# Performance work log

Measured on AMD Instinct MI355X. Metric: run time of the kernel, lower is better.

## Reference

```python
import jax, jax.numpy as jnp
import numpy as np

N = 8192
IN_F = 512
OUT_F = 512
ALPHA = 0.2  # leaky relu slope


def setup_inputs() -> dict:
    key = jax.random.key(0)
    k1, k2, k3, k4, k5 = jax.random.split(key, 5)
    inp = jax.random.normal(k1, (N, IN_F), dtype=jnp.float32)
    adj = jax.random.randint(k2, (N, N), 0, 2, dtype=jnp.int32)
    # linear1: [in, out] + bias
    W1 = jax.random.normal(k3, (IN_F, OUT_F), dtype=jnp.float32) * (1.0 / np.sqrt(IN_F))
    b1 = jnp.zeros((OUT_F,), dtype=jnp.float32)
    # linear2: maps 2*out -> 1; split into the two halves acting on h_i and h_j
    a = jax.random.normal(k4, (2 * OUT_F,), dtype=jnp.float32) * (1.0 / np.sqrt(2 * OUT_F))
    a1 = a[:OUT_F]
    a2 = a[OUT_F:]
    b2 = jnp.zeros((), dtype=jnp.float32)
    return {"inp": inp, "adj": adj, "W1": W1, "b1": b1, "a1": a1, "a2": a2, "b2": b2}


def reference(inp, adj, W1, b1, a1, a2, b2):
    h = inp @ W1 + b1  # [N, out]
    # linear2(cat(h_i, h_j)) == h_i@a1 + h_j@a2 + b2 -> avoids the N*N*2F tensor
    e = jax.nn.leaky_relu((h @ a1)[:, None] + (h @ a2)[None, :] + b2, ALPHA)  # [N, N]
    attention = jnp.where(adj > 0, e, jnp.float32(-1e12))
    attention = jax.nn.softmax(attention, axis=1)
    h_prime = attention @ h  # [N, out]
    return jax.nn.elu(h_prime)  # concat=True
```

## Files before the change

kernel.cpp:

```cpp
#include <hip/hip_runtime.h>
#include <hip/hip_bf16.h>
#include <stdint.h>

#define NR 8192
#define FD 512
#define BM 64

typedef __attribute__((ext_vector_type(8))) short s8v;
typedef __attribute__((ext_vector_type(4))) float f32x4;

static __device__ __forceinline__ short bf16_rtne(float x) {
    union { float f; uint32_t u; } v; v.f = x;
    uint32_t r = (v.u + 0x7FFFu + ((v.u >> 16) & 1u)) >> 16;
    return (short)r;
}
static __device__ __forceinline__ float bf16_to_f32(short s) {
    union { uint32_t u; float f; } v; v.u = ((uint32_t)(uint16_t)s) << 16;
    return v.f;
}

__global__ void k_prep(const float* __restrict__ in, short* __restrict__ out,
                       const float* __restrict__ W1, short* __restrict__ W1T) {
    int b = blockIdx.x;
    if (b < 4096) {
        int i = b * 256 + threadIdx.x;
        float4 v = ((const float4*)in)[i];
        short4 s;
        s.x = bf16_rtne(v.x); s.y = bf16_rtne(v.y);
        s.z = bf16_rtne(v.z); s.w = bf16_rtne(v.w);
        ((short4*)out)[i] = s;
    } else {
        int i = (b - 4096) * 256 + threadIdx.x;
        int k = i & 511, n = i >> 9;
        W1T[(size_t)n * 512 + k] = bf16_rtne(W1[(size_t)k * 512 + n]);
    }
}

__launch_bounds__(256)
__global__ void k_gemm_h(const short* __restrict__ A,
                         const short* __restrict__ BT,
                         const float* __restrict__ b1,
                         short* __restrict__ H,
                         short* __restrict__ HT3)
{
    const int lane = threadIdx.x & 63;
    const int wn   = threadIdx.x >> 6;
    const int m    = lane & 15;
    const int q    = lane >> 4;
    const int r0   = blockIdx.x * 32;
    const int c0   = blockIdx.y * 128 + wn * 32;

    f32x4 acc[2][2] = {};
#pragma unroll 1
    for (int k0 = 0; k0 < 512; k0 += 32) {
        s8v a[2], b[2];
#pragma unroll
        for (int rt = 0; rt < 2; ++rt)
            a[rt] = *(const s8v*)(A + (size_t)(r0 + rt * 16 + m) * 512 + k0 + q * 8);
#pragma unroll
        for (int nt = 0; nt < 2; ++nt)
            b[nt] = *(const s8v*)(BT + (size_t)(c0 + nt * 16 + m) * 512 + k0 + q * 8);
#pragma unroll
        for (int rt = 0; rt < 2; ++rt)
#pragma unroll
            for (int nt = 0; nt < 2; ++nt)
                acc[rt][nt] = __builtin_amdgcn_mfma_f32_16x16x32_bf16(a[rt], b[nt], acc[rt][nt], 0, 0, 0);
    }
    float b1v[2];
#pragma unroll
    for (int nt = 0; nt < 2; ++nt) b1v[nt] = b1[c0 + nt * 16 + m];

#pragma unroll
    for (int rt = 0; rt < 2; ++rt)
#pragma unroll
        for (int nt = 0; nt < 2; ++nt) {
            int col = c0 + nt * 16 + m;
            short4 hp;
#pragma unroll
            for (int r = 0; r < 4; ++r) {
                int row = r0 + rt * 16 + q * 4 + r;
                short hv = bf16_rtne(acc[rt][nt][r] + b1v[nt]);
                H[(size_t)row * 512 + col] = hv;
                ((short*)&hp)[r] = hv;
            }
            size_t off = (size_t)blockIdx.x * 16384
                       + (size_t)(blockIdx.y * 2 + (wn >> 1)) * 2048
                       + (size_t)((wn * 2 + nt) & 3) * 512
                       + (rt * 2 + (q >> 1)) * 128
                       + m * 8 + (q & 1) * 4;
            *(short4*)(HT3 + off) = hp;
        }
}

__global__ void k_f1f2(const short* __restrict__ H, const float* __restrict__ a1,
                       const float* __restrict__ a2, const float* __restrict__ b2,
                       float* __restrict__ f1, float* __restrict__ f2s)
{
    const int lane = threadIdx.x & 63;
    const int row  = blockIdx.x * 4 + (threadIdx.x >> 6);
    s8v hv = *(const s8v*)(H + (size_t)row * 512 + lane * 8);
    float4 a1l = ((const float4*)(a1 + lane * 8))[0];
    float4 a1h = ((const float4*)(a1 + lane * 8))[1];
    float4 a2l = ((const float4*)(a2 + lane * 8))[0];
    float4 a2h = ((const float4*)(a2 + lane * 8))[1];
    float hf[8];
#pragma unroll
    for (int i = 0; i < 8; ++i) hf[i] = bf16_to_f32(hv[i]);
    float s1 = hf[0] * a1l.x + hf[1] * a1l.y + hf[2] * a1l.z + hf[3] * a1l.w
             + hf[4] * a1h.x + hf[5] * a1h.y + hf[6] * a1h.z + hf[7] * a1h.w;
    float s2 = hf[0] * a2l.x + hf[1] * a2l.y + hf[2] * a2l.z + hf[3] * a2l.w
             + hf[4] * a2h.x + hf[5] * a2h.y + hf[6] * a2h.z + hf[7] * a2h.w;
#pragma unroll
    for (int o = 32; o > 0; o >>= 1) {
        s1 += __shfl_xor(s1, o);
        s2 += __shfl_xor(s2, o);
    }
    if (lane == 0) {
        f1[row]  = s1;
        f2s[row] = s2 + b2[0];
    }
}

__launch_bounds__(1024, 4)
__global__ void k_attn(const int* __restrict__ adj,
                       const short* __restrict__ HT3,
                       const float* __restrict__ f1,
                       const float* __restrict__ f2s,
                       float* __restrict__ nump,
                       float* __restrict__ denomp)
{
    __shared__ __align__(16) short wt[2][BM * 256];

    const int t    = threadIdx.x;
    const int lane = t & 63;
    const int w    = t >> 6;
    const int m    = lane & 15;
    const int q    = lane >> 4;

    const int js   = blockIdx.x & 1;
    const int band = blockIdx.x >> 1;
    const int r0   = band * BM;
    const int jb0  = js * 4096;
    const int jt0  = js * 128;

    const int prow = t >> 4;
    const int jg   = t & 15;

    const float f1v = f1[r0 + prow];
    const int* adjrow = adj + (size_t)(r0 + prow) * NR + jb0;
    const float* f2base = f2s + jb0;

    f32x4 acc[4][2] = {};
    float dsum = 0.f;

#define GAT_BLOAD(DST, KT)                                                     \
    {                                                                          \
        const short* s_ = HT3 + (size_t)(jt0 + (KT)) * 16384 + (w >> 1) * 2048 \
                        + (w & 1) * 1024 + q * 128 + m * 8;                    \
        DST[0] = *(const s8v*)(s_);                                            \
        DST[1] = *(const s8v*)(s_ + 512);                                      \
    }

#define GAT_MLOAD(DST, AP, U)                                                  \
    {                                                                          \
        uint4 ma_ = *(const uint4*)((AP) + (U) * 8);                           \
        uint4 mb_ = *(const uint4*)((AP) + (U) * 8 + 4);                       \
        DST = ((int)ma_.x > 0 ? 1u : 0u)  | ((int)ma_.y > 0 ? 2u : 0u)         \
            | ((int)ma_.z > 0 ? 4u : 0u)  | ((int)ma_.w > 0 ? 8u : 0u)         \
            | ((int)mb_.x > 0 ? 16u : 0u) | ((int)mb_.y > 0 ? 32u : 0u)        \
            | ((int)mb_.z > 0 ? 64u : 0u) | ((int)mb_.w > 0 ? 128u : 0u);      \
    }

#define GAT_WUNIT(U, BYTE, FA, FB, P)                                          \
    {                                                                          \
        s8v wv_;                                                               \
        const float* ff_ = (const float*)&(FA);                                \
        _Pragma("unroll")                                                      \
        for (int jj = 0; jj < 4; ++jj) {                                       \
            float s_ = f1v + ff_[jj];                                          \
            float e_ = __expf(fmaxf(s_, 0.2f * s_));                           \
            float x_ = (((BYTE) >> jj) & 1u) ? e_ : 0.f;                       \
            dsum += x_; wv_[jj] = bf16_rtne(x_);                               \
        }                                                                      \
        const float* fg_ = (const float*)&(FB);                               \
        _Pragma("unroll")                                                      \
        for (int jj = 0; jj < 4; ++jj) {                                       \
            float s_ = f1v + fg_[jj];                                          \
            float e_ = __expf(fmaxf(s_, 0.2f * s_));                           \
            float x_ = (((BYTE) >> (4 + jj)) & 1u) ? e_ : 0.f;                 \
            dsum += x_; wv_[4 + jj] = bf16_rtne(x_);                           \
        }                                                                      \
        *(s8v*)&wt[P][prow * 256 + (((U) ^ (prow & 7)) << 3)] = wv_;           \
    }

    {
#pragma unroll
        for (int k_ = 0; k_ < 2; ++k_) {
            const int u_ = jg + 16 * k_;
            uint32_t mk_;
            GAT_MLOAD(mk_, adjrow, u_)
            float4 fa_ = *(const float4*)(f2base + u_ * 8);
            float4 fb_ = *(const float4*)(f2base + u_ * 8 + 4);
            GAT_WUNIT(u_, mk_, fa_, fb_, 0)
        }
    }
    s8v breg[2][2];
    GAT_BLOAD(breg[0], 0)
    GAT_BLOAD(breg[1], 1)
    __syncthreads();

    int kt = 0;
#pragma unroll 1
    for (int ch = 0; ch < 16; ++ch) {
        const int p = ch & 1;
        const int chn = (ch + 1) & 15;
        const int* adjn = adjrow + chn * 256;
        const float* f2n = f2base + chn * 256;
        uint32_t mkn_[2];
        float4 fan_[2], fbn_[2];

#pragma unroll
        for (int kk = 0; kk < 8; ++kk, ++kt) {
            const int e = kk & 1;
            s8v bn[2];
            GAT_BLOAD(bn, (kt + 2) & 127)
            if (kk < 2 && ch < 15) {
                const int u_ = jg + 16 * kk;
                GAT_MLOAD(mkn_[kk], adjn, u_)
                fan_[kk] = *(const float4*)(f2n + u_ * 8);
                fbn_[kk] = *(const float4*)(f2n + u_ * 8 + 4);
            }
            s8v af[4];
#pragma unroll
            for (int i = 0; i < 4; ++i)
                af[i] = *(const s8v*)&wt[p][(i * 16 + m) * 256
                                            + (((kk * 4 + q) ^ (m & 7)) << 3)];
#pragma unroll
            for (int nt = 0; nt < 2; ++nt)
#pragma unroll
                for (int i = 0; i < 4; ++i)
                    acc[i][nt] = __builtin_amdgcn_mfma_f32_16x16x32_bf16(af[i], breg[e][nt], acc[i][nt], 0, 0, 0);
            if (kk >= 4 && kk <= 5 && ch < 15) {
                const int k_ = kk - 4;
                const int u_ = jg + 16 * k_;
                GAT_WUNIT(u_, mkn_[k_], fan_[k_], fbn_[k_], p ^ 1)
            }
#pragma unroll
            for (int nt = 0; nt < 2; ++nt) breg[e][nt] = bn[nt];
        }
        __syncthreads();
    }
#undef GAT_BLOAD
#undef GAT_MLOAD
#undef GAT_WUNIT

    dsum += __shfl_xor(dsum, 1);
    dsum += __shfl_xor(dsum, 2);
    dsum += __shfl_xor(dsum, 4);
    dsum += __shfl_xor(dsum, 8);
    if (jg == 0) denomp[(size_t)js * NR + r0 + prow] = dsum;

    float* np = nump + (size_t)js * NR * FD;
#pragma unroll
    for (int i = 0; i < 4; ++i)
#pragma unroll
        for (int nt = 0; nt < 2; ++nt)
#pragma unroll
            for (int r = 0; r < 4; ++r) {
                int row = r0 + i * 16 + q * 4 + r;
                int col = w * 32 + nt * 16 + m;
                np[(size_t)row * FD + col] = acc[i][nt][r];
            }
}

__global__ void k_combine(const float* __restrict__ nump,
                          const float* __restrict__ denomp,
                          float* __restrict__ out)
{
    size_t e = ((size_t)blockIdx.x * 256 + threadIdx.x) * 4;
    int row = (int)(e >> 9);
    float4 n0 = *(const float4*)(nump + e);
    float4 n1 = *(const float4*)(nump + (size_t)NR * FD + e);
    float d = denomp[row] + denomp[NR + row];
    float inv = 1.0f / d;
    float4 o;
    o.x = (n0.x + n1.x) * inv;
    o.y = (n0.y + n1.y) * inv;
    o.z = (n0.z + n1.z) * inv;
    o.w = (n0.w + n1.w) * inv;
    o.x = (o.x > 0.f) ? o.x : (__expf(o.x) - 1.f);
    o.y = (o.y > 0.f) ? o.y : (__expf(o.y) - 1.f);
    o.z = (o.z > 0.f) ? o.z : (__expf(o.z) - 1.f);
    o.w = (o.w > 0.f) ? o.w : (__expf(o.w) - 1.f);
    *(float4*)(out + e) = o;
}

extern "C" void kernel_launch(void* const* d_in, const int* in_sizes, int n_in,
                              void* d_out, int out_size, void* d_ws, size_t ws_size,
                              hipStream_t stream) {
    const float* inp = (const float*)d_in[0];
    const int*   adj = (const int*)d_in[1];
    const float* W1  = (const float*)d_in[2];
    const float* b1  = (const float*)d_in[3];
    const float* a1  = (const float*)d_in[4];
    const float* a2  = (const float*)d_in[5];
    const float* b2  = (const float*)d_in[6];
    float* out = (float*)d_out;

    short*    inp_bf = (short*)d_ws;
    short*    w1t    = inp_bf + (size_t)NR * FD;
    short*    h      = w1t + (size_t)FD * FD;
    short*    ht3    = h + (size_t)NR * FD;
    float*    f1     = (float*)(ht3 + (size_t)FD * NR);
    float*    f2s    = f1 + NR;
    float*    nump   = f2s + NR;
    float*    denomp = nump + (size_t)2 * NR * FD;

    k_prep<<<4096 + 1024, 256, 0, stream>>>(inp, inp_bf, W1, w1t);
    dim3 g1(NR / 32, FD / 128);
    k_gemm_h<<<g1, 256, 0, stream>>>(inp_bf, w1t, b1, h, ht3);
    k_f1f2<<<NR / 4, 256, 0, stream>>>(h, a1, a2, b2, f1, f2s);
    k_attn<<<128 * 2, 1024, 0, stream>>>(adj, ht3, f1, f2s, nump, denomp);
    k_combine<<<(NR * FD / 4) / 256, 256, 0, stream>>>(nump, denomp, out);
}
```

Baseline: 459.7 us.

## Split attention into separate weight-generation and GEMM kernels via global bf16 buffer

The fused attention kernel is split in two. A new k_wgen kernel reads the adjacency matrix, computes the masked exp weights in bf16 in a pre-swizzled layout, and writes them to a global N×N workspace along with the full per-row denominator. k_agemm then streams those weights into shared memory and runs only the MFMA GEMM. This takes the exp and mask work off the GEMM's critical path and spreads it across many small blocks. In exchange it adds a 128 MB bf16 write plus a read-back through HBM and one extra kernel launch.

```diff
diff --git a/kernel.cpp b/kernel.cpp
--- a/kernel.cpp
+++ b/kernel.cpp
@@ -4,7 +4,6 @@
 
 #define NR 8192
 #define FD 512
-#define BM 64
 
 typedef __attribute__((ext_vector_type(8))) short s8v;
 typedef __attribute__((ext_vector_type(4))) float f32x4;
@@ -121,15 +120,92 @@
     }
 }
 
-__launch_bounds__(1024, 4)
-__global__ void k_attn(const int* __restrict__ adj,
-                       const short* __restrict__ HT3,
+__launch_bounds__(256)
+__global__ void k_wgen(const int* __restrict__ adj,
                        const float* __restrict__ f1,
                        const float* __restrict__ f2s,
-                       float* __restrict__ nump,
+                       short* __restrict__ wsw,
                        float* __restrict__ denomp)
 {
-    __shared__ __align__(16) short wt[2][BM * 256];
+    const int t    = threadIdx.x;
+    const int prow = t >> 5;
+    const int jg   = t & 31;
+    const int row  = blockIdx.x * 8 + prow;
+    const int band = row >> 6;
+    const int prow64 = row & 63;
+
+    const float f1v = f1[row];
+    const int* adjrow = adj + (size_t)row * NR;
+    short* wbase = wsw + ((size_t)(band * 32) * 64 + prow64) * 256
+                 + ((jg ^ (prow64 & 7)) << 3);
+
+    float dsum = 0.f;
+
+#define WG_COMPUTE(CH, MA, MB, FA, FB)                                         \
+    {                                                                          \
+        uint32_t bm_ =                                                         \
+              ((int)(MA).x > 0 ? 1u : 0u)   | ((int)(MA).y > 0 ? 2u : 0u)      \
+            | ((int)(MA).z > 0 ? 4u : 0u)   | ((int)(MA).w > 0 ? 8u : 0u)      \
+            | ((int)(MB).x > 0 ? 16u : 0u)  | ((int)(MB).y > 0 ? 32u : 0u)     \
+            | ((int)(MB).z > 0 ? 64u : 0u)  | ((int)(MB).w > 0 ? 128u : 0u);   \
+        s8v wv_;                                                               \
+        const float* ff_ = (const float*)&(FA);                                \
+        _Pragma("unroll")                                                      \
+        for (int jj = 0; jj < 4; ++jj) {                                       \
+            float s_ = f1v + ff_[jj];                                          \
+            float e_ = __expf(fmaxf(s_, 0.2f * s_));                           \
+            float x_ = ((bm_ >> jj) & 1u) ? e_ : 0.f;                          \
+            dsum += x_; wv_[jj] = bf16_rtne(x_);                               \
+        }                                                                      \
+        const float* fg_ = (const float*)&(FB);                                \
+        _Pragma("unroll")                                                      \
+        for (int jj = 0; jj < 4; ++jj) {                                       \
+            float s_ = f1v + fg_[jj];                                          \
+            float e_ = __expf(fmaxf(s_, 0.2f * s_));                           \
+            float x_ = ((bm_ >> (4 + jj)) & 1u) ? e_ : 0.f;                    \
+            dsum += x_; wv_[4 + jj] = bf16_rtne(x_);                           \
+        }                                                                      \
+        *(s8v*)(wbase + (size_t)(CH) * 16384) = wv_;                           \
+    }
+
+    uint4 ca, cb; float4 cf0, cf1;
+    ca  = *(const uint4*)(adjrow + jg * 8);
+    cb  = *(const uint4*)(adjrow + jg * 8 + 4);
+    cf0 = *(const float4*)(f2s + jg * 8);
+    cf1 = *(const float4*)(f2s + jg * 8 + 4);
+#pragma unroll 1
+    for (int c2 = 0; c2 < 16; ++c2) {
+        const int ch = c2 * 2;
+        uint4 na, nb; float4 nf0, nf1;
+        na  = *(const uint4*)(adjrow + (ch + 1) * 256 + jg * 8);
+        nb  = *(const uint4*)(adjrow + (ch + 1) * 256 + jg * 8 + 4);
+        nf0 = *(const float4*)(f2s + (ch + 1) * 256 + jg * 8);
+        nf1 = *(const float4*)(f2s + (ch + 1) * 256 + jg * 8 + 4);
+        WG_COMPUTE(ch, ca, cb, cf0, cf1)
+        if (c2 < 15) {
+            ca  = *(const uint4*)(adjrow + (ch + 2) * 256 + jg * 8);
+            cb  = *(const uint4*)(adjrow + (ch + 2) * 256 + jg * 8 + 4);
+            cf0 = *(const float4*)(f2s + (ch + 2) * 256 + jg * 8);
+            cf1 = *(const float4*)(f2s + (ch + 2) * 256 + jg * 8 + 4);
+        }
+        WG_COMPUTE(ch + 1, na, nb, nf0, nf1)
+    }
+#undef WG_COMPUTE
+
+    dsum += __shfl_xor(dsum, 1);
+    dsum += __shfl_xor(dsum, 2);
+    dsum += __shfl_xor(dsum, 4);
+    dsum += __shfl_xor(dsum, 8);
+    dsum += __shfl_xor(dsum, 16);
+    if (jg == 0) denomp[row] = dsum;
+}
+
+__launch_bounds__(1024, 4)
+__global__ void k_agemm(const short* __restrict__ WSW,
+                        const short* __restrict__ HT3,
+                        float* __restrict__ nump)
+{
+    __shared__ __align__(16) short wt[2][16384];
 
     const int t    = threadIdx.x;
     const int lane = t & 63;
@@ -139,19 +215,10 @@
 
     const int js   = blockIdx.x & 1;
     const int band = blockIdx.x >> 1;
-    const int r0   = band * BM;
-    const int jb0  = js * 4096;
+    const int r0   = band * 64;
     const int jt0  = js * 128;
 
-    const int prow = t >> 4;
-    const int jg   = t & 15;
-
-    const float f1v = f1[r0 + prow];
-    const int* adjrow = adj + (size_t)(r0 + prow) * NR + jb0;
-    const float* f2base = f2s + jb0;
-
     f32x4 acc[4][2] = {};
-    float dsum = 0.f;
 
 #define GAT_BLOAD(DST, KT)                                                     \
     {                                                                          \
@@ -161,48 +228,13 @@
         DST[1] = *(const s8v*)(s_ + 512);                                      \
     }
 
-#define GAT_MLOAD(DST, AP, U)                                                  \
-    {                                                                          \
-        uint4 ma_ = *(const uint4*)((AP) + (U) * 8);                           \
-        uint4 mb_ = *(const uint4*)((AP) + (U) * 8 + 4);                       \
-        DST = ((int)ma_.x > 0 ? 1u : 0u)  | ((int)ma_.y > 0 ? 2u : 0u)         \
-            | ((int)ma_.z > 0 ? 4u : 0u)  | ((int)ma_.w > 0 ? 8u : 0u)         \
-            | ((int)mb_.x > 0 ? 16u : 0u) | ((int)mb_.y > 0 ? 32u : 0u)        \
-            | ((int)mb_.z > 0 ? 64u : 0u) | ((int)mb_.w > 0 ? 128u : 0u);      \
-    }
-
-#define GAT_WUNIT(U, BYTE, FA, FB, P)                                          \
-    {                                                                          \
-        s8v wv_;                                                               \
-        const float* ff_ = (const float*)&(FA);                                \
-        _Pragma("unroll")                                                      \
-        for (int jj = 0; jj < 4; ++jj) {                                       \
-            float s_ = f1v + ff_[jj];                                          \
-            float e_ = __expf(fmaxf(s_, 0.2f * s_));                           \
-            float x_ = (((BYTE) >> jj) & 1u) ? e_ : 0.f;                       \
-            dsum += x_; wv_[jj] = bf16_rtne(x_);                               \
-        }                                                                      \
-        const float* fg_ = (const float*)&(FB);                               \
-        _Pragma("unroll")                                                      \
-        for (int jj = 0; jj < 4; ++jj) {                                       \
-            float s_ = f1v + fg_[jj];                                          \
-            float e_ = __expf(fmaxf(s_, 0.2f * s_));                           \
-            float x_ = (((BYTE) >> (4 + jj)) & 1u) ? e_ : 0.f;                 \
-            dsum += x_; wv_[4 + jj] = bf16_rtne(x_);                           \
-        }                                                                      \
-        *(s8v*)&wt[P][prow * 256 + (((U) ^ (prow & 7)) << 3)] = wv_;           \
-    }
+    const short* wsrc = WSW + (size_t)(band * 32 + js * 16) * 16384;
 
     {
-#pragma unroll
-        for (int k_ = 0; k_ < 2; ++k_) {
-            const int u_ = jg + 16 * k_;
-            uint32_t mk_;
-            GAT_MLOAD(mk_, adjrow, u_)
-            float4 fa_ = *(const float4*)(f2base + u_ * 8);
-            float4 fb_ = *(const float4*)(f2base + u_ * 8 + 4);
-            GAT_WUNIT(u_, mk_, fa_, fb_, 0)
-        }
+        s8v s0 = *(const s8v*)(wsrc + t * 16);
+        s8v s1 = *(const s8v*)(wsrc + t * 16 + 8);
+        *(s8v*)&wt[0][t * 16]     = s0;
+        *(s8v*)&wt[0][t * 16 + 8] = s1;
     }
     s8v breg[2][2];
     GAT_BLOAD(breg[0], 0)
@@ -213,23 +245,18 @@
 #pragma unroll 1
     for (int ch = 0; ch < 16; ++ch) {
         const int p = ch & 1;
-        const int chn = (ch + 1) & 15;
-        const int* adjn = adjrow + chn * 256;
-        const float* f2n = f2base + chn * 256;
-        uint32_t mkn_[2];
-        float4 fan_[2], fbn_[2];
+        s8v sg0, sg1;
+        if (ch < 15) {
+            const short* ws = wsrc + (size_t)(ch + 1) * 16384;
+            sg0 = *(const s8v*)(ws + t * 16);
+            sg1 = *(const s8v*)(ws + t * 16 + 8);
+        }
 
 #pragma unroll
         for (int kk = 0; kk < 8; ++kk, ++kt) {
             const int e = kk & 1;
             s8v bn[2];
             GAT_BLOAD(bn, (kt + 2) & 127)
-            if (kk < 2 && ch < 15) {
-                const int u_ = jg + 16 * kk;
-                GAT_MLOAD(mkn_[kk], adjn, u_)
-                fan_[kk] = *(const float4*)(f2n + u_ * 8);
-                fbn_[kk] = *(const float4*)(f2n + u_ * 8 + 4);
-            }
             s8v af[4];
 #pragma unroll
             for (int i = 0; i < 4; ++i)
@@ -240,25 +267,16 @@
 #pragma unroll
                 for (int i = 0; i < 4; ++i)
                     acc[i][nt] = __builtin_amdgcn_mfma_f32_16x16x32_bf16(af[i], breg[e][nt], acc[i][nt], 0, 0, 0);
-            if (kk >= 4 && kk <= 5 && ch < 15) {
-                const int k_ = kk - 4;
-                const int u_ = jg + 16 * k_;
-                GAT_WUNIT(u_, mkn_[k_], fan_[k_], fbn_[k_], p ^ 1)
-            }
 #pragma unroll
             for (int nt = 0; nt < 2; ++nt) breg[e][nt] = bn[nt];
         }
+        if (ch < 15) {
+            *(s8v*)&wt[p ^ 1][t * 16]     = sg0;
+            *(s8v*)&wt[p ^ 1][t * 16 + 8] = sg1;
+        }
         __syncthreads();
     }
 #undef GAT_BLOAD
-#undef GAT_MLOAD
-#undef GAT_WUNIT
-
-    dsum += __shfl_xor(dsum, 1);
-    dsum += __shfl_xor(dsum, 2);
-    dsum += __shfl_xor(dsum, 4);
-    dsum += __shfl_xor(dsum, 8);
-    if (jg == 0) denomp[(size_t)js * NR + r0 + prow] = dsum;
 
     float* np = nump + (size_t)js * NR * FD;
 #pragma unroll
@@ -281,7 +299,7 @@
     int row = (int)(e >> 9);
     float4 n0 = *(const float4*)(nump + e);
     float4 n1 = *(const float4*)(nump + (size_t)NR * FD + e);
-    float d = denomp[row] + denomp[NR + row];
+    float d = denomp[row];
     float inv = 1.0f / d;
     float4 o;
     o.x = (n0.x + n1.x) * inv;
@@ -313,13 +331,15 @@
     short*    ht3    = h + (size_t)NR * FD;
     float*    f1     = (float*)(ht3 + (size_t)FD * NR);
     float*    f2s    = f1 + NR;
-    float*    nump   = f2s + NR;
+    short*    wsw    = (short*)(f2s + NR);
+    float*    nump   = (float*)(wsw + (size_t)NR * NR);
     float*    denomp = nump + (size_t)2 * NR * FD;
 
     k_prep<<<4096 + 1024, 256, 0, stream>>>(inp, inp_bf, W1, w1t);
     dim3 g1(NR / 32, FD / 128);
     k_gemm_h<<<g1, 256, 0, stream>>>(inp_bf, w1t, b1, h, ht3);
     k_f1f2<<<NR / 4, 256, 0, stream>>>(h, a1, a2, b2, f1, f2s);
-    k_attn<<<128 * 2, 1024, 0, stream>>>(adj, ht3, f1, f2s, nump, denomp);
+    k_wgen<<<NR / 8, 256, 0, stream>>>(adj, f1, f2s, wsw, denomp);
+    k_agemm<<<128 * 2, 1024, 0, stream>>>(wsw, ht3, nump);
     k_combine<<<(NR * FD / 4) / 256, 256, 0, stream>>>(nump, denomp, out);
 }
```

Result: slower. 531.9 us (+15.7%).
